# Performance work log

Hardware: AMD Instinct MI355X
Metric: run time of the kernel (lower is better)

Reference implementation:

```python
import jax, jax.numpy as jnp
import numpy as np
import math
from jax import lax

B, T, GS = 16, 511, 1
OBS, OUT = 60, 30
D, H, L = 1024, 16, 8
DFF, HID = 4096, 100
S = T + GS
DH = D // H
EPS = 1e-5


def _ln(x, g, b):
    m = jnp.mean(x, axis=-1, keepdims=True)
    v = jnp.mean(jnp.square(x - m), axis=-1, keepdims=True)
    return (x - m) * lax.rsqrt(v + EPS) * g + b


def setup_inputs():
    key = jax.random.key(0)
    ks = iter(jax.random.split(key, 32))
    def n(shape):
        return jax.random.normal(next(ks), shape, dtype=jnp.float32) * 0.02
    return {
        "states": jax.random.normal(next(ks), (B, T, OBS), dtype=jnp.float32),
        "goals": jax.random.normal(next(ks), (B, GS, OBS), dtype=jnp.float32),
        "Wtok": n((OBS, D)), "btok": jnp.zeros((D,), jnp.float32),
        "pos": n((1, S, D)),
        "ln1_g": jnp.ones((L, D), jnp.float32), "ln1_b": jnp.zeros((L, D), jnp.float32),
        "Wq": n((L, D, D)), "bq": jnp.zeros((L, D), jnp.float32),
        "Wk": n((L, D, D)), "bk": jnp.zeros((L, D), jnp.float32),
        "Wv": n((L, D, D)), "bv": jnp.zeros((L, D), jnp.float32),
        "Wp": n((L, D, D)), "bp": jnp.zeros((L, D), jnp.float32),
        "ln2_g": jnp.ones((L, D), jnp.float32), "ln2_b": jnp.zeros((L, D), jnp.float32),
        "Wm1": n((L, D, DFF)), "bm1": jnp.zeros((L, DFF), jnp.float32),
        "Wm2": n((L, DFF, D)), "bm2": jnp.zeros((L, D), jnp.float32),
        "lnf_g": jnp.ones((D,), jnp.float32), "lnf_b": jnp.zeros((D,), jnp.float32),
        "Wh1": n((D, HID)), "bh1": jnp.zeros((HID,), jnp.float32),
        "Wh2": n((HID, OUT)), "bh2": jnp.zeros((OUT,), jnp.float32),
    }


def reference(states, goals, Wtok, btok, pos, ln1_g, ln1_b, Wq, bq, Wk, bk, Wv, bv, Wp, bp,
              ln2_g, ln2_b, Wm1, bm1, Wm2, bm2, lnf_g, lnf_b, Wh1, bh1, Wh2, bh2):
    # token + positional embeddings (dropout is identity in eval mode, pdrop=0)
    goal_x = goals @ Wtok + btok + pos[:, :GS]
    state_x = states @ Wtok + btok + pos[:, GS:S]
    x = jnp.concatenate([goal_x, state_x], axis=1)  # (B, S, D)
    mask = jnp.tril(jnp.ones((S, S), dtype=bool))
    scale = 1.0 / math.sqrt(DH)

    def block(x, p):
        g1, b1, wq, bq_, wk, bk_, wv, bv_, wp, bp_, g2, b2, w1, bm1_, w2, bm2_ = p
        h = _ln(x, g1, b1)
        q = (h @ wq + bq_).reshape(B, S, H, DH).transpose(0, 2, 1, 3)  # (B,H,S,DH)
        k = (h @ wk + bk_).reshape(B, S, H, DH).transpose(0, 2, 1, 3)
        v = (h @ wv + bv_).reshape(B, S, H, DH).transpose(0, 2, 1, 3)
        att = jnp.einsum('bhqd,bhkd->bhqk', q, k) * scale
        att = jnp.where(mask, att, -jnp.inf)
        att = jax.nn.softmax(att, axis=-1)
        y = jnp.einsum('bhqk,bhkd->bhqd', att, v)
        y = y.transpose(0, 2, 1, 3).reshape(B, S, D) @ wp + bp_
        x = x + y
        h = _ln(x, g2, b2)
        x = x + (jax.nn.gelu(h @ w1 + bm1_, approximate=False) @ w2 + bm2_)
        return x, None

    x, _ = lax.scan(block, x, (ln1_g, ln1_b, Wq, bq, Wk, bk, Wv, bv, Wp, bp,
                               ln2_g, ln2_b, Wm1, bm1, Wm2, bm2))
    x = _ln(x, lnf_g, lnf_b)[:, GS:]  # drop goal tokens -> (B, T, D)
    h = jax.nn.silu(x @ Wh1 + bh1)
    return h @ Wh2 + bh2
```

## Files before the change

### kernel.cpp

```cpp
#include <hip/hip_runtime.h>
#include <cstdint>
#include <math.h>

#define NB_B   16
#define NB_T   511
#define NB_S   512
#define NB_OBS 60
#define NB_D   1024
#define NB_H   16
#define NB_L   8
#define NB_DFF 4096
#define NB_HID 100
#define NB_OUT 30
#define NB_M   8192
#define QKV_S  3072

typedef __attribute__((ext_vector_type(8))) short  short8;
typedef __attribute__((ext_vector_type(4))) short  short4v;
typedef __attribute__((ext_vector_type(4))) float  f32x4;
typedef __attribute__((ext_vector_type(8))) __bf16 bf16x8;

template <int N_> struct ic { static constexpr int v = N_; };

__device__ __forceinline__ short f2bf(float f) {
  union { float f; unsigned u; } a; a.f = f;
  unsigned u = a.u + 0x7fffu + ((a.u >> 16) & 1u);
  return (short)(u >> 16);
}

__device__ __forceinline__ void load_lds16(const void* g, void* l) {
  __builtin_amdgcn_global_load_lds(
      (__attribute__((address_space(1))) unsigned int*)(uintptr_t)g,
      (__attribute__((address_space(3))) unsigned int*)(unsigned)(uintptr_t)l,
      16, 0, 0);
}

__device__ __forceinline__ f32x4 mfma16(short8 a, short8 b, f32x4 c) {
  return __builtin_amdgcn_mfma_f32_16x16x32_bf16(
      __builtin_bit_cast(bf16x8, a), __builtin_bit_cast(bf16x8, b), c, 0, 0, 0);
}

__device__ __forceinline__ float gelu_fast(float v) {
  const float t = 1.5957691216057308f * (v + 0.044715f * v * v * v);
  const float e = __expf(fminf(t, 30.f));
  return v * (e / (e + 1.f));
}

__global__ __launch_bounds__(256) void tconv2_kernel(
    const float* __restrict__ src, short* __restrict__ dst,
    int R, int C, size_t sstride, size_t dstride) {
  __shared__ float t[64][65];
  const float* s0 = src + blockIdx.z * sstride;
  short* d0 = dst + blockIdx.z * dstride;
  const int c0 = blockIdx.x * 64, r0 = blockIdx.y * 64;
#pragma unroll
  for (int i = 0; i < 4; i++) {
    const int idx = threadIdx.x + i * 256;
    const int r = idx >> 4, c4 = (idx & 15) * 4;
    const float4 v = *(const float4*)&s0[(size_t)(r0 + r) * C + c0 + c4];
    t[r][c4 + 0] = v.x; t[r][c4 + 1] = v.y; t[r][c4 + 2] = v.z; t[r][c4 + 3] = v.w;
  }
  __syncthreads();
#pragma unroll
  for (int i = 0; i < 2; i++) {
    const int idx = threadIdx.x + i * 256;
    const int c = idx >> 3, g = (idx & 7) * 8;
    short8 o;
#pragma unroll
    for (int j = 0; j < 8; j++) o[j] = f2bf(t[g + j][c]);
    *(short8*)&d0[(size_t)(c0 + c) * R + r0 + g] = o;
  }
}

__global__ __launch_bounds__(256) void whead_prep(
    const float* __restrict__ Wh1, const float* __restrict__ bh1,
    short* __restrict__ Wh1t, float* __restrict__ bh1p) {
  const int idx = blockIdx.x * 256 + threadIdx.x;
  const int n = idx >> 10, k = idx & 1023;
  Wh1t[idx] = (n < NB_HID) ? f2bf(Wh1[k * NB_HID + n]) : (short)0;
  if (idx < 128) bh1p[idx] = (idx < NB_HID) ? bh1[idx] : 0.f;
}

__global__ __launch_bounds__(256) void qkvbias_prep(
    const float* __restrict__ bq, const float* __restrict__ bk,
    const float* __restrict__ bv, float* __restrict__ outb) {
  const int idx = blockIdx.x * 256 + threadIdx.x;
  const int l = idx / QKV_S, r = idx - l * QKV_S;
  const int z = r >> 10, c = r & 1023;
  const float* src = (z == 0) ? bq : ((z == 1) ? bk : bv);
  outb[idx] = src[l * NB_D + c];
}

__global__ __launch_bounds__(256) void embed2_kernel(
    const float* __restrict__ states, const float* __restrict__ goals,
    const float* __restrict__ Wtok, const float* __restrict__ btok,
    const float* __restrict__ pos, float* __restrict__ x) {
  const int r0 = blockIdx.x * 8;
  __shared__ float tok[8][NB_OBS];
  for (int idx = threadIdx.x; idx < 8 * NB_OBS; idx += 256) {
    const int r = idx / NB_OBS, o = idx - r * NB_OBS;
    const int row = r0 + r, b = row >> 9, s = row & 511;
    tok[r][o] = (s == 0) ? goals[b * NB_OBS + o]
                         : states[((size_t)b * NB_T + (s - 1)) * NB_OBS + o];
  }
  __syncthreads();
#pragma unroll
  for (int i = 0; i < 4; i++) {
    const int d = threadIdx.x + i * 256;
    float acc[8];
#pragma unroll
    for (int r = 0; r < 8; r++) acc[r] = 0.f;
    for (int o = 0; o < NB_OBS; o++) {
      const float wv = Wtok[o * NB_D + d];
#pragma unroll
      for (int r = 0; r < 8; r++) acc[r] += tok[r][o] * wv;
    }
    const float bt = btok[d];
#pragma unroll
    for (int r = 0; r < 8; r++) {
      const int row = r0 + r, s = row & 511;
      x[(size_t)row * NB_D + d] = acc[r] + bt + pos[(size_t)s * NB_D + d];
    }
  }
}

template <typename OutT>
__global__ __launch_bounds__(256) void ln_wave(
    const float* __restrict__ xin, const float* __restrict__ gam,
    const float* __restrict__ bet, OutT* __restrict__ outp) {
  const int row = blockIdx.x * 4 + (threadIdx.x >> 6);
  const int lane = threadIdx.x & 63;
  const float4* src = (const float4*)(xin + (size_t)row * NB_D);
  float4 v[4];
  float s = 0.f, s2 = 0.f;
#pragma unroll
  for (int i = 0; i < 4; i++) {
    v[i] = src[lane + 64 * i];
    s += v[i].x + v[i].y + v[i].z + v[i].w;
    s2 += v[i].x * v[i].x + v[i].y * v[i].y + v[i].z * v[i].z + v[i].w * v[i].w;
  }
#pragma unroll
  for (int o = 32; o; o >>= 1) {
    s += __shfl_xor(s, o, 64);
    s2 += __shfl_xor(s2, o, 64);
  }
  const float mean = s * (1.f / NB_D);
  const float var = s2 * (1.f / NB_D) - mean * mean;
  const float rs = rsqrtf(var + 1e-5f);
#pragma unroll
  for (int i = 0; i < 4; i++) {
    const float4 g4 = ((const float4*)gam)[lane + 64 * i];
    const float4 b4 = ((const float4*)bet)[lane + 64 * i];
    const float o0 = (v[i].x - mean) * rs * g4.x + b4.x;
    const float o1 = (v[i].y - mean) * rs * g4.y + b4.y;
    const float o2 = (v[i].z - mean) * rs * g4.z + b4.z;
    const float o3 = (v[i].w - mean) * rs * g4.w + b4.w;
    if constexpr (sizeof(OutT) == 2) {
      short4v r = {f2bf(o0), f2bf(o1), f2bf(o2), f2bf(o3)};
      *(short4v*)((short*)outp + (size_t)row * NB_D + (lane + 64 * i) * 4) = r;
    } else {
      ((float4*)((float*)outp + (size_t)row * NB_D))[lane + 64 * i] =
          make_float4(o0, o1, o2, o3);
    }
  }
}

template <int ACT, bool RESID, typename OutT>
__global__ __launch_bounds__(256) void gemm_bt(
    const short* __restrict__ A, const short* __restrict__ Bt,
    const float* __restrict__ bias, const float* __restrict__ resid,
    OutT* __restrict__ C, int N, int K) {
  __shared__ short As[128][32];
  __shared__ short Bs[128][32];
  const int bm = blockIdx.y * 128, bn = blockIdx.x * 128;
  const int tid = threadIdx.x;
  const int w = tid >> 6, lane = tid & 63;
  const int wr = (w >> 1) * 64, wc = (w & 1) * 64;
  const int rr = lane & 15, sg = lane >> 4;

  f32x4 acc[4][4];
#pragma unroll
  for (int i = 0; i < 4; i++)
#pragma unroll
    for (int j = 0; j < 4; j++) acc[i][j] = f32x4{0.f, 0.f, 0.f, 0.f};

  const int srow0 = w * 32 + (lane >> 2);
  const int sslot = lane & 3;

  for (int k0 = 0; k0 < K; k0 += 32) {
    __syncthreads();
#pragma unroll
    for (int inst = 0; inst < 2; inst++) {
      const int r = srow0 + inst * 16;
      const int sl = sslot ^ ((r >> 1) & 3);
      load_lds16(A + (size_t)(bm + r) * K + k0 + sl * 8, &As[w * 32 + inst * 16][0]);
      load_lds16(Bt + (size_t)(bn + r) * K + k0 + sl * 8, &Bs[w * 32 + inst * 16][0]);
    }
    __syncthreads();
    short8 a[4], b[4];
#pragma unroll
    for (int i = 0; i < 4; i++) {
      const int r = wr + i * 16 + rr;
      a[i] = *(const short8*)&As[r][(sg ^ ((r >> 1) & 3)) * 8];
      const int c = wc + i * 16 + rr;
      b[i] = *(const short8*)&Bs[c][(sg ^ ((c >> 1) & 3)) * 8];
    }
#pragma unroll
    for (int i = 0; i < 4; i++)
#pragma unroll
      for (int j = 0; j < 4; j++) acc[i][j] = mfma16(a[i], b[j], acc[i][j]);
  }

#pragma unroll
  for (int j = 0; j < 4; j++) {
    const int col = bn + wc + j * 16 + rr;
    const float bv = bias[col];
#pragma unroll
    for (int i = 0; i < 4; i++) {
#pragma unroll
      for (int q = 0; q < 4; q++) {
        const int row = bm + wr + i * 16 + sg * 4 + q;
        float v = acc[i][j][q] + bv;
        if constexpr (RESID) v += resid[(size_t)row * N + col];
        if constexpr (ACT == 1) v = gelu_fast(v);
        if constexpr (ACT == 2) v = v / (1.f + __expf(-v));
        if constexpr (sizeof(OutT) == 2) C[(size_t)row * N + col] = (OutT)f2bf(v);
        else C[(size_t)row * N + col] = v;
      }
    }
  }
}

template <int BM, int N, int K, int ACT, bool RESID, typename OutT>
__device__ __forceinline__ void gemmv4_core(
    const short* __restrict__ A, const short* __restrict__ Bt,
    const float* __restrict__ bias, const float* __restrict__ resid,
    OutT* __restrict__ C) {
  constexpr int MI = BM / 32;
  constexpr int NK = K / 32;
  constexpr int NBN = N / 128;
  constexpr int NWG = (NB_M / BM) * NBN;
  constexpr int QC = NWG / 8;
  constexpr int L = 2 + BM / 64;
  constexpr int SA = BM * 32;

  __shared__ short As[3][SA];
  __shared__ short Bs[3][128 * 32];

  int wg = blockIdx.x;
  wg = (wg & 7) * QC + (wg >> 3);
  const int bm = (wg / NBN) * BM;
  const int bn = (wg % NBN) * 128;

  const int tid = threadIdx.x;
  const int w = tid >> 6, lane = tid & 63;
  const int wm = w >> 1, wn = w & 1;
  const int rr = lane & 15, sg = lane >> 4;
  const int lrow = lane >> 2, lslot = lane & 3;
  const int sslot = lslot ^ ((lrow >> 1) & 3);

  const short* Asrc = A + (size_t)(bm + w * 16 + lrow) * K + sslot * 8;
  const short* Bsrc = Bt + (size_t)(bn + w * 16 + lrow) * K + sslot * 8;
  short* Adst = &As[0][w * 512];
  short* Bdst = &Bs[0][w * 512];

  const int ar = wm * (BM / 2) + rr;
  const int br = wn * 64 + rr;
  const int aoff = ar * 32 + ((sg ^ ((ar >> 1) & 3)) * 8);
  const int boff = br * 32 + ((sg ^ ((br >> 1) & 3)) * 8);

  f32x4 acc[MI][4];
#pragma unroll
  for (int i = 0; i < MI; i++)
#pragma unroll
    for (int j = 0; j < 4; j++) acc[i][j] = f32x4{0.f, 0.f, 0.f, 0.f};

  auto stage = [&](int sb, int k0) {
    load_lds16(Bsrc + k0,                  Bdst + sb * 4096);
    load_lds16(Bsrc + (size_t)64 * K + k0, Bdst + sb * 4096 + 2048);
#pragma unroll
    for (int c = 0; c < BM / 64; c++)
      load_lds16(Asrc + (size_t)(c * 64) * K + k0, Adst + sb * SA + c * 2048);
  };

  auto gate = [&]() {
    if constexpr (L == 6) asm volatile("s_waitcnt vmcnt(6)" ::: "memory");
    else                  asm volatile("s_waitcnt vmcnt(4)" ::: "memory");
  };

  stage(0, 0);
  stage(1, 32);
  gate();
  __builtin_amdgcn_s_barrier();

  auto ktile = [&](auto BUFC, auto SBUFC, int t) {
    constexpr int BUF = decltype(BUFC)::v;
    constexpr int SBUF = decltype(SBUFC)::v;
    const short* Ab = &As[BUF][0];
    const short* Bb = &Bs[BUF][0];
    if (t + 2 < NK) stage(SBUF, (t + 2) * 32);
    short8 a[MI], b[4];
#pragma unroll
    for (int i = 0; i < MI; i++) a[i] = *(const short8*)(Ab + aoff + i * 512);
#pragma unroll
    for (int j = 0; j < 4; j++) b[j] = *(const short8*)(Bb + boff + j * 512);
    __builtin_amdgcn_s_setprio(1);
#pragma unroll
    for (int i = 0; i < MI; i++)
#pragma unroll
      for (int j = 0; j < 4; j++) acc[i][j] = mfma16(a[i], b[j], acc[i][j]);
    __builtin_amdgcn_s_setprio(0);
    if (t + 2 < NK)      gate();
    else if (t + 1 < NK) asm volatile("s_waitcnt vmcnt(0)" ::: "memory");
    __builtin_amdgcn_s_barrier();
  };

  int t = 0;
#pragma unroll 1
  for (; t + 3 <= NK; t += 3) {
    ktile(ic<0>{}, ic<2>{}, t);
    ktile(ic<1>{}, ic<0>{}, t + 1);
    ktile(ic<2>{}, ic<1>{}, t + 2);
  }
  if constexpr (NK % 3 >= 1) ktile(ic<0>{}, ic<2>{}, NK - NK % 3);
  if constexpr (NK % 3 >= 2) ktile(ic<1>{}, ic<0>{}, NK - NK % 3 + 1);

  const int col0 = bn + wn * 64 + rr;
  float bv[4];
#pragma unroll
  for (int j = 0; j < 4; j++) bv[j] = bias[col0 + j * 16];
#pragma unroll
  for (int i = 0; i < MI; i++) {
#pragma unroll
    for (int q = 0; q < 4; q++) {
      const size_t row = bm + wm * (BM / 2) + i * 16 + sg * 4 + q;
      float v0 = acc[i][0][q] + bv[0];
      float v1 = acc[i][1][q] + bv[1];
      float v2 = acc[i][2][q] + bv[2];
      float v3 = acc[i][3][q] + bv[3];
      if constexpr (RESID) {
        const float* rrow = resid + row * N + col0;
        v0 += rrow[0]; v1 += rrow[16]; v2 += rrow[32]; v3 += rrow[48];
      }
      if constexpr (ACT == 1) {
        v0 = gelu_fast(v0); v1 = gelu_fast(v1);
        v2 = gelu_fast(v2); v3 = gelu_fast(v3);
      }
      OutT* crow = C + row * N + col0;
      if constexpr (sizeof(OutT) == 2) {
        crow[0] = (OutT)f2bf(v0); crow[16] = (OutT)f2bf(v1);
        crow[32] = (OutT)f2bf(v2); crow[48] = (OutT)f2bf(v3);
      } else {
        crow[0] = v0; crow[16] = v1; crow[32] = v2; crow[48] = v3;
      }
    }
  }
}

template <int BM, int N, int K, int ACT, bool RESID, typename OutT>
__global__ __launch_bounds__(256, 2) void gemmv4(
    const short* __restrict__ A, const short* __restrict__ Bt,
    const float* __restrict__ bias, const float* __restrict__ resid,
    OutT* __restrict__ C) {
  gemmv4_core<BM, N, K, ACT, RESID, OutT>(A, Bt, bias, resid, C);
}

__global__ __launch_bounds__(256) void attn_kernel(
    const short* __restrict__ qkv, short* __restrict__ out) {
  const int qt = blockIdx.x, hh = blockIdx.y, bb = blockIdx.z;
  const int tid = threadIdx.x;
  const int w = tid >> 6, lane = tid & 63;
  const int rr = lane & 15, sg = lane >> 4;

  __shared__ short Ks[64][64];
  __shared__ short Vt[64][64];
  __shared__ short Ps[4][16][64];

  short8 qf[2];
  {
    const size_t qrow = (size_t)bb * NB_S + qt * 64 + w * 16 + rr;
#pragma unroll
    for (int ks = 0; ks < 2; ks++)
      qf[ks] = *(const short8*)&qkv[qrow * QKV_S + hh * 64 + ks * 32 + sg * 8];
  }

  float mrow[4], lrow[4];
  f32x4 o[4];
#pragma unroll
  for (int j = 0; j < 4; j++) { mrow[j] = -INFINITY; lrow[j] = 0.f; }
#pragma unroll
  for (int nb = 0; nb < 4; nb++) o[nb] = f32x4{0.f, 0.f, 0.f, 0.f};

  for (int kt = 0; kt <= qt; kt++) {
    __syncthreads();
    {
      const int p = lane & 7;
#pragma unroll
      for (int inst = 0; inst < 2; inst++) {
        const int r = w * 16 + inst * 8 + (lane >> 3);
        const int sl = p ^ (r & 7);
        load_lds16(qkv + ((size_t)bb * NB_S + kt * 64 + r) * QKV_S + 1024 + hh * 64 + sl * 8,
                   &Ks[w * 16 + inst * 8][0]);
      }
    }
    {
#pragma unroll
      for (int cc = 0; cc < 2; cc++) {
        const int c = tid * 2 + cc;
        const int sk = c >> 3, sl = c & 7;
        short8 vv = *(const short8*)&qkv[((size_t)bb * NB_S + kt * 64 + sk) * QKV_S + 2048 + hh * 64 + sl * 8];
        const int ss = sk >> 3;
#pragma unroll
        for (int j = 0; j < 8; j++) {
          const int dh = sl * 8 + j;
          Vt[dh][(ss ^ (dh & 7)) * 8 + (sk & 7)] = vv[j];
        }
      }
    }
    __syncthreads();

    f32x4 sf[4];
#pragma unroll
    for (int nb = 0; nb < 4; nb++) sf[nb] = f32x4{0.f, 0.f, 0.f, 0.f};
#pragma unroll
    for (int ks = 0; ks < 2; ks++) {
#pragma unroll
      for (int nb = 0; nb < 4; nb++) {
        const int ck = nb * 16 + rr;
        short8 kf = *(const short8*)&Ks[ck][((ks * 4 + sg) ^ (ck & 7)) * 8];
        sf[nb] = mfma16(qf[ks], kf, sf[nb]);
      }
    }
    const int rbase = qt * 64 + w * 16 + sg * 4;
    float pmax[4] = {-INFINITY, -INFINITY, -INFINITY, -INFINITY};
#pragma unroll
    for (int nb = 0; nb < 4; nb++) {
      const int cg = kt * 64 + nb * 16 + rr;
#pragma unroll
      for (int j = 0; j < 4; j++) {
        float sv = sf[nb][j] * 0.125f;
        if (cg > rbase + j) sv = -INFINITY;
        sf[nb][j] = sv;
        pmax[j] = fmaxf(pmax[j], sv);
      }
    }
#pragma unroll
    for (int o1 = 1; o1 < 16; o1 <<= 1)
#pragma unroll
      for (int j = 0; j < 4; j++)
        pmax[j] = fmaxf(pmax[j], __shfl_xor(pmax[j], o1, 64));

    float resc[4], psum[4];
#pragma unroll
    for (int j = 0; j < 4; j++) {
      const float mn = fmaxf(mrow[j], pmax[j]);
      resc[j] = __expf(mrow[j] - mn);
      mrow[j] = mn;
      psum[j] = 0.f;
    }
#pragma unroll
    for (int nb = 0; nb < 4; nb++)
#pragma unroll
      for (int j = 0; j < 4; j++) {
        const float p = __expf(sf[nb][j] - mrow[j]);
        sf[nb][j] = p;
        psum[j] += p;
      }
#pragma unroll
    for (int o1 = 1; o1 < 16; o1 <<= 1)
#pragma unroll
      for (int j = 0; j < 4; j++) psum[j] += __shfl_xor(psum[j], o1, 64);
#pragma unroll
    for (int j = 0; j < 4; j++) lrow[j] = lrow[j] * resc[j] + psum[j];
#pragma unroll
    for (int nb = 0; nb < 4; nb++)
#pragma unroll
      for (int j = 0; j < 4; j++) o[nb][j] *= resc[j];

#pragma unroll
    for (int nb = 0; nb < 4; nb++) {
      const int ck = nb * 16 + rr;
      const int ss = ck >> 3;
#pragma unroll
      for (int j = 0; j < 4; j++) {
        const int rq = sg * 4 + j;
        Ps[w][rq][(ss ^ (rq & 7)) * 8 + (ck & 7)] = f2bf(sf[nb][j]);
      }
    }
#pragma unroll
    for (int ks = 0; ks < 2; ks++) {
      short8 pf = *(const short8*)&Ps[w][rr][((ks * 4 + sg) ^ (rr & 7)) * 8];
#pragma unroll
      for (int nb = 0; nb < 4; nb++) {
        const int dh = nb * 16 + rr;
        short8 vf = *(const short8*)&Vt[dh][((ks * 4 + sg) ^ (dh & 7)) * 8];
        o[nb] = mfma16(pf, vf, o[nb]);
      }
    }
  }

  {
    const size_t orow0 = (size_t)bb * NB_S + qt * 64 + w * 16;
#pragma unroll
    for (int nb = 0; nb < 4; nb++)
#pragma unroll
      for (int j = 0; j < 4; j++) {
        const float v = o[nb][j] / lrow[j];
        out[(orow0 + sg * 4 + j) * NB_D + hh * 64 + nb * 16 + rr] = f2bf(v);
      }
  }
}

__global__ __launch_bounds__(256) void head2_kernel(
    const float* __restrict__ hbuf, const float* __restrict__ Wh2,
    const float* __restrict__ bh2, float* __restrict__ outp) {
  __shared__ float hs[8][NB_HID];
  const int g0 = blockIdx.x * 8;
  for (int idx = threadIdx.x; idx < 8 * NB_HID; idx += 256) {
    const int r = idx / NB_HID, k = idx - r * NB_HID;
    const int gt = g0 + r;
    const int b = gt / NB_T, tt = gt - b * NB_T;
    hs[r][k] = hbuf[(size_t)(b * NB_S + 1 + tt) * 128 + k];
  }
  __syncthreads();
  const int r = threadIdx.x >> 5, c = threadIdx.x & 31;
  if (c < NB_OUT) {
    float acc = bh2[c];
#pragma unroll
    for (int k = 0; k < NB_HID; k++) acc += hs[r][k] * Wh2[k * NB_OUT + c];
    outp[(size_t)(g0 + r) * NB_OUT + c] = acc;
  }
}

extern "C" void kernel_launch(void* const* d_in, const int* in_sizes, int n_in,
                              void* d_out, int out_size, void* d_ws, size_t ws_size,
                              hipStream_t stream) {
  const float* states = (const float*)d_in[0];
  const float* goals  = (const float*)d_in[1];
  const float* Wtok   = (const float*)d_in[2];
  const float* btok   = (const float*)d_in[3];
  const float* pos    = (const float*)d_in[4];
  const float* ln1_g  = (const float*)d_in[5];
  const float* ln1_b  = (const float*)d_in[6];
  const float* Wq     = (const float*)d_in[7];
  const float* bq     = (const float*)d_in[8];
  const float* Wk     = (const float*)d_in[9];
  const float* bk     = (const float*)d_in[10];
  const float* Wv     = (const float*)d_in[11];
  const float* bv     = (const float*)d_in[12];
  const float* Wp     = (const float*)d_in[13];
  const float* bp     = (const float*)d_in[14];
  const float* ln2_g  = (const float*)d_in[15];
  const float* ln2_b  = (const float*)d_in[16];
  const float* Wm1    = (const float*)d_in[17];
  const float* bm1    = (const float*)d_in[18];
  const float* Wm2    = (const float*)d_in[19];
  const float* bm2    = (const float*)d_in[20];
  const float* lnf_g  = (const float*)d_in[21];
  const float* lnf_b  = (const float*)d_in[22];
  const float* Wh1    = (const float*)d_in[23];
  const float* bh1    = (const float*)d_in[24];
  const float* Wh2    = (const float*)d_in[25];
  const float* bh2    = (const float*)d_in[26];

  char* wsp = (char*)d_ws;
  size_t off = 0;
  auto carve = [&](size_t bytes) -> char* {
    char* p = wsp + off;
    off += (bytes + 1023) & ~(size_t)1023;
    return p;
  };
  short* Wqkv_t = (short*)carve((size_t)NB_L * 3 * NB_D * NB_D * 2);
  short* Wp_t   = (short*)carve((size_t)NB_L * NB_D * NB_D * 2);
  short* Wm1_t  = (short*)carve((size_t)NB_L * NB_DFF * NB_D * 2);
  short* Wm2_t  = (short*)carve((size_t)NB_L * NB_D * NB_DFF * 2);
  float* x      = (float*)carve((size_t)NB_M * NB_D * 4);
  short* h      = (short*)carve((size_t)NB_M * NB_D * 2);
  short* qkvb   = (short*)carve((size_t)NB_M * QKV_S * 2);
  short* mlp    = (short*)carve((size_t)NB_M * NB_DFF * 2);
  short* Wh1t   = (short*)carve((size_t)128 * NB_D * 2);
  float* bh1p   = (float*)carve(128 * 4);
  float* bqkv   = (float*)carve((size_t)NB_L * QKV_S * 4);
  short* attout = mlp;
  float* hbuf   = (float*)qkvb;

  const dim3 thr(256);
  const size_t DD = (size_t)NB_D * NB_D;
  const size_t DF = (size_t)NB_D * NB_DFF;

  tconv2_kernel<<<dim3(16, 16, NB_L), thr, 0, stream>>>(Wq, Wqkv_t + 0 * DD, NB_D, NB_D, DD, 3 * DD);
  tconv2_kernel<<<dim3(16, 16, NB_L), thr, 0, stream>>>(Wk, Wqkv_t + 1 * DD, NB_D, NB_D, DD, 3 * DD);
  tconv2_kernel<<<dim3(16, 16, NB_L), thr, 0, stream>>>(Wv, Wqkv_t + 2 * DD, NB_D, NB_D, DD, 3 * DD);
  tconv2_kernel<<<dim3(16, 16, NB_L), thr, 0, stream>>>(Wp, Wp_t, NB_D, NB_D, DD, DD);
  tconv2_kernel<<<dim3(64, 16, NB_L), thr, 0, stream>>>(Wm1, Wm1_t, NB_D, NB_DFF, DF, DF);
  tconv2_kernel<<<dim3(16, 64, NB_L), thr, 0, stream>>>(Wm2, Wm2_t, NB_DFF, NB_D, DF, DF);
  whead_prep<<<512, thr, 0, stream>>>(Wh1, bh1, Wh1t, bh1p);
  qkvbias_prep<<<96, thr, 0, stream>>>(bq, bk, bv, bqkv);

  embed2_kernel<<<NB_M / 8, thr, 0, stream>>>(states, goals, Wtok, btok, pos, x);

  for (int l = 0; l < NB_L; l++) {
    ln_wave<short><<<NB_M / 4, thr, 0, stream>>>(x, ln1_g + l * NB_D, ln1_b + l * NB_D, h);
    gemmv4<256, QKV_S, NB_D, 0, false, short><<<768, thr, 0, stream>>>(
        h, Wqkv_t + (size_t)l * 3 * DD, bqkv + (size_t)l * QKV_S, nullptr, qkvb);
    attn_kernel<<<dim3(NB_S / 64, NB_H, NB_B), thr, 0, stream>>>(qkvb, attout);
    gemmv4<128, NB_D, NB_D, 0, true, float><<<512, thr, 0, stream>>>(
        attout, Wp_t + (size_t)l * DD, bp + l * NB_D, x, x);
    ln_wave<short><<<NB_M / 4, thr, 0, stream>>>(x, ln2_g + l * NB_D, ln2_b + l * NB_D, h);
    gemmv4<256, NB_DFF, NB_D, 1, false, short><<<1024, thr, 0, stream>>>(
        h, Wm1_t + (size_t)l * DF, bm1 + l * NB_DFF, nullptr, mlp);
    gemmv4<128, NB_D, NB_DFF, 0, true, float><<<512, thr, 0, stream>>>(
        mlp, Wm2_t + (size_t)l * DF, bm2 + l * NB_D, x, x);
  }

  ln_wave<short><<<NB_M / 4, thr, 0, stream>>>(x, lnf_g, lnf_b, h);
  gemm_bt<2, false, float><<<dim3(1, NB_M / 128), thr, 0, stream>>>(
      h, Wh1t, bh1p, nullptr, hbuf, 128, NB_D);
  head2_kernel<<<NB_M / 8, thr, 0, stream>>>(hbuf, Wh2, bh2, (float*)d_out);
}
```

Measured before the change: 2.872 ms.

## Process 128 query rows per attention block to reuse K/V tiles

```diff
diff --git a/kernel.cpp b/kernel.cpp
--- a/kernel.cpp
+++ b/kernel.cpp
@@ -165,6 +165,140 @@
   }
 }
 
+template <int BM, int N, int K, int ACT, bool RESID, typename OutT>
+__device__ __forceinline__ void gemmv4_core(
+    const short* __restrict__ A, const short* __restrict__ Bt,
+    const float* __restrict__ bias, const float* __restrict__ resid,
+    OutT* __restrict__ C) {
+  constexpr int MI = BM / 32;
+  constexpr int NK = K / 32;
+  constexpr int NBN = N / 128;
+  constexpr int NWG = (NB_M / BM) * NBN;
+  constexpr int QC = NWG / 8;
+  constexpr int L = 2 + BM / 64;
+  constexpr int SA = BM * 32;
+
+  __shared__ short As[3][SA];
+  __shared__ short Bs[3][128 * 32];
+
+  int wg = blockIdx.x;
+  wg = (wg & 7) * QC + (wg >> 3);
+  const int bm = (wg / NBN) * BM;
+  const int bn = (wg % NBN) * 128;
+
+  const int tid = threadIdx.x;
+  const int w = tid >> 6, lane = tid & 63;
+  const int wm = w >> 1, wn = w & 1;
+  const int rr = lane & 15, sg = lane >> 4;
+  const int lrow = lane >> 2, lslot = lane & 3;
+  const int sslot = lslot ^ ((lrow >> 1) & 3);
+
+  const short* Asrc = A + (size_t)(bm + w * 16 + lrow) * K + sslot * 8;
+  const short* Bsrc = Bt + (size_t)(bn + w * 16 + lrow) * K + sslot * 8;
+  short* Adst = &As[0][w * 512];
+  short* Bdst = &Bs[0][w * 512];
+
+  const int ar = wm * (BM / 2) + rr;
+  const int br = wn * 64 + rr;
+  const int aoff = ar * 32 + ((sg ^ ((ar >> 1) & 3)) * 8);
+  const int boff = br * 32 + ((sg ^ ((br >> 1) & 3)) * 8);
+
+  f32x4 acc[MI][4];
+#pragma unroll
+  for (int i = 0; i < MI; i++)
+#pragma unroll
+    for (int j = 0; j < 4; j++) acc[i][j] = f32x4{0.f, 0.f, 0.f, 0.f};
+
+  auto stage = [&](int sb, int k0) {
+    load_lds16(Bsrc + k0,                  Bdst + sb * 4096);
+    load_lds16(Bsrc + (size_t)64 * K + k0, Bdst + sb * 4096 + 2048);
+#pragma unroll
+    for (int c = 0; c < BM / 64; c++)
+      load_lds16(Asrc + (size_t)(c * 64) * K + k0, Adst + sb * SA + c * 2048);
+  };
+
+  auto gate = [&]() {
+    if constexpr (L == 6) asm volatile("s_waitcnt vmcnt(6)" ::: "memory");
+    else                  asm volatile("s_waitcnt vmcnt(4)" ::: "memory");
+  };
+
+  stage(0, 0);
+  stage(1, 32);
+  gate();
+  __builtin_amdgcn_s_barrier();
+
+  auto ktile = [&](auto BUFC, auto SBUFC, int t) {
+    constexpr int BUF = decltype(BUFC)::v;
+    constexpr int SBUF = decltype(SBUFC)::v;
+    const short* Ab = &As[BUF][0];
+    const short* Bb = &Bs[BUF][0];
+    if (t + 2 < NK) stage(SBUF, (t + 2) * 32);
+    short8 a[MI], b[4];
+#pragma unroll
+    for (int i = 0; i < MI; i++) a[i] = *(const short8*)(Ab + aoff + i * 512);
+#pragma unroll
+    for (int j = 0; j < 4; j++) b[j] = *(const short8*)(Bb + boff + j * 512);
+    __builtin_amdgcn_s_setprio(1);
+#pragma unroll
+    for (int i = 0; i < MI; i++)
+#pragma unroll
+      for (int j = 0; j < 4; j++) acc[i][j] = mfma16(a[i], b[j], acc[i][j]);
+    __builtin_amdgcn_s_setprio(0);
+    if (t + 2 < NK)      gate();
+    else if (t + 1 < NK) asm volatile("s_waitcnt vmcnt(0)" ::: "memory");
+    __builtin_amdgcn_s_barrier();
+  };
+
+  int t = 0;
+#pragma unroll 1
+  for (; t + 3 <= NK; t += 3) {
+    ktile(ic<0>{}, ic<2>{}, t);
+    ktile(ic<1>{}, ic<0>{}, t + 1);
+    ktile(ic<2>{}, ic<1>{}, t + 2);
+  }
+  if constexpr (NK % 3 >= 1) ktile(ic<0>{}, ic<2>{}, NK - NK % 3);
+  if constexpr (NK % 3 >= 2) ktile(ic<1>{}, ic<0>{}, NK - NK % 3 + 1);
+
+  const int col0 = bn + wn * 64 + rr;
+  float bv[4];
+#pragma unroll
+  for (int j = 0; j < 4; j++) bv[j] = bias[col0 + j * 16];
+#pragma unroll
+  for (int i = 0; i < MI; i++) {
+#pragma unroll
+    for (int q = 0; q < 4; q++) {
+      const size_t row = bm + wm * (BM / 2) + i * 16 + sg * 4 + q;
+      float v0 = acc[i][0][q] + bv[0];
+      float v1 = acc[i][1][q] + bv[1];
+      float v2 = acc[i][2][q] + bv[2];
+      float v3 = acc[i][3][q] + bv[3];
+      if constexpr (RESID) {
+        const float* rrow = resid + row * N + col0;
+        v0 += rrow[0]; v1 += rrow[16]; v2 += rrow[32]; v3 += rrow[48];
+      }
+      if constexpr (ACT == 1) {
+        v0 = gelu_fast(v0); v1 = gelu_fast(v1);
+        v2 = gelu_fast(v2); v3 = gelu_fast(v3);
+      }
+      OutT* crow = C + row * N + col0;
+      if constexpr (sizeof(OutT) == 2) {
+        crow[0] = (OutT)f2bf(v0); crow[16] = (OutT)f2bf(v1);
+        crow[32] = (OutT)f2bf(v2); crow[48] = (OutT)f2bf(v3);
+      } else {
+        crow[0] = v0; crow[16] = v1; crow[32] = v2; crow[48] = v3;
+      }
+    }
+  }
+}
+
+template <int BM, int N, int K, int ACT, bool RESID, typename OutT>
+__global__ __launch_bounds__(256, 2) void gemmv4(
+    const short* __restrict__ A, const short* __restrict__ Bt,
+    const float* __restrict__ bias, const float* __restrict__ resid,
+    OutT* __restrict__ C) {
+  gemmv4_core<BM, N, K, ACT, RESID, OutT>(A, Bt, bias, resid, C);
+}
+
 template <int ACT, bool RESID, typename OutT>
 __global__ __launch_bounds__(256) void gemm_bt(
     const short* __restrict__ A, const short* __restrict__ Bt,
@@ -231,141 +365,7 @@
   }
 }
 
-template <int BM, int N, int K, int ACT, bool RESID, typename OutT>
-__device__ __forceinline__ void gemmv4_core(
-    const short* __restrict__ A, const short* __restrict__ Bt,
-    const float* __restrict__ bias, const float* __restrict__ resid,
-    OutT* __restrict__ C) {
-  constexpr int MI = BM / 32;
-  constexpr int NK = K / 32;
-  constexpr int NBN = N / 128;
-  constexpr int NWG = (NB_M / BM) * NBN;
-  constexpr int QC = NWG / 8;
-  constexpr int L = 2 + BM / 64;
-  constexpr int SA = BM * 32;
-
-  __shared__ short As[3][SA];
-  __shared__ short Bs[3][128 * 32];
-
-  int wg = blockIdx.x;
-  wg = (wg & 7) * QC + (wg >> 3);
-  const int bm = (wg / NBN) * BM;
-  const int bn = (wg % NBN) * 128;
-
-  const int tid = threadIdx.x;
-  const int w = tid >> 6, lane = tid & 63;
-  const int wm = w >> 1, wn = w & 1;
-  const int rr = lane & 15, sg = lane >> 4;
-  const int lrow = lane >> 2, lslot = lane & 3;
-  const int sslot = lslot ^ ((lrow >> 1) & 3);
-
-  const short* Asrc = A + (size_t)(bm + w * 16 + lrow) * K + sslot * 8;
-  const short* Bsrc = Bt + (size_t)(bn + w * 16 + lrow) * K + sslot * 8;
-  short* Adst = &As[0][w * 512];
-  short* Bdst = &Bs[0][w * 512];
-
-  const int ar = wm * (BM / 2) + rr;
-  const int br = wn * 64 + rr;
-  const int aoff = ar * 32 + ((sg ^ ((ar >> 1) & 3)) * 8);
-  const int boff = br * 32 + ((sg ^ ((br >> 1) & 3)) * 8);
-
-  f32x4 acc[MI][4];
-#pragma unroll
-  for (int i = 0; i < MI; i++)
-#pragma unroll
-    for (int j = 0; j < 4; j++) acc[i][j] = f32x4{0.f, 0.f, 0.f, 0.f};
-
-  auto stage = [&](int sb, int k0) {
-    load_lds16(Bsrc + k0,                  Bdst + sb * 4096);
-    load_lds16(Bsrc + (size_t)64 * K + k0, Bdst + sb * 4096 + 2048);
-#pragma unroll
-    for (int c = 0; c < BM / 64; c++)
-      load_lds16(Asrc + (size_t)(c * 64) * K + k0, Adst + sb * SA + c * 2048);
-  };
-
-  auto gate = [&]() {
-    if constexpr (L == 6) asm volatile("s_waitcnt vmcnt(6)" ::: "memory");
-    else                  asm volatile("s_waitcnt vmcnt(4)" ::: "memory");
-  };
-
-  stage(0, 0);
-  stage(1, 32);
-  gate();
-  __builtin_amdgcn_s_barrier();
-
-  auto ktile = [&](auto BUFC, auto SBUFC, int t) {
-    constexpr int BUF = decltype(BUFC)::v;
-    constexpr int SBUF = decltype(SBUFC)::v;
-    const short* Ab = &As[BUF][0];
-    const short* Bb = &Bs[BUF][0];
-    if (t + 2 < NK) stage(SBUF, (t + 2) * 32);
-    short8 a[MI], b[4];
-#pragma unroll
-    for (int i = 0; i < MI; i++) a[i] = *(const short8*)(Ab + aoff + i * 512);
-#pragma unroll
-    for (int j = 0; j < 4; j++) b[j] = *(const short8*)(Bb + boff + j * 512);
-    __builtin_amdgcn_s_setprio(1);
-#pragma unroll
-    for (int i = 0; i < MI; i++)
-#pragma unroll
-      for (int j = 0; j < 4; j++) acc[i][j] = mfma16(a[i], b[j], acc[i][j]);
-    __builtin_amdgcn_s_setprio(0);
-    if (t + 2 < NK)      gate();
-    else if (t + 1 < NK) asm volatile("s_waitcnt vmcnt(0)" ::: "memory");
-    __builtin_amdgcn_s_barrier();
-  };
-
-  int t = 0;
-#pragma unroll 1
-  for (; t + 3 <= NK; t += 3) {
-    ktile(ic<0>{}, ic<2>{}, t);
-    ktile(ic<1>{}, ic<0>{}, t + 1);
-    ktile(ic<2>{}, ic<1>{}, t + 2);
-  }
-  if constexpr (NK % 3 >= 1) ktile(ic<0>{}, ic<2>{}, NK - NK % 3);
-  if constexpr (NK % 3 >= 2) ktile(ic<1>{}, ic<0>{}, NK - NK % 3 + 1);
-
-  const int col0 = bn + wn * 64 + rr;
-  float bv[4];
-#pragma unroll
-  for (int j = 0; j < 4; j++) bv[j] = bias[col0 + j * 16];
-#pragma unroll
-  for (int i = 0; i < MI; i++) {
-#pragma unroll
-    for (int q = 0; q < 4; q++) {
-      const size_t row = bm + wm * (BM / 2) + i * 16 + sg * 4 + q;
-      float v0 = acc[i][0][q] + bv[0];
-      float v1 = acc[i][1][q] + bv[1];
-      float v2 = acc[i][2][q] + bv[2];
-      float v3 = acc[i][3][q] + bv[3];
-      if constexpr (RESID) {
-        const float* rrow = resid + row * N + col0;
-        v0 += rrow[0]; v1 += rrow[16]; v2 += rrow[32]; v3 += rrow[48];
-      }
-      if constexpr (ACT == 1) {
-        v0 = gelu_fast(v0); v1 = gelu_fast(v1);
-        v2 = gelu_fast(v2); v3 = gelu_fast(v3);
-      }
-      OutT* crow = C + row * N + col0;
-      if constexpr (sizeof(OutT) == 2) {
-        crow[0] = (OutT)f2bf(v0); crow[16] = (OutT)f2bf(v1);
-        crow[32] = (OutT)f2bf(v2); crow[48] = (OutT)f2bf(v3);
-      } else {
-        crow[0] = v0; crow[16] = v1; crow[32] = v2; crow[48] = v3;
-      }
-    }
-  }
-}
-
-template <int BM, int N, int K, int ACT, bool RESID, typename OutT>
-__global__ __launch_bounds__(256, 2) void gemmv4(
-    const short* __restrict__ A, const short* __restrict__ Bt,
-    const float* __restrict__ bias, const float* __restrict__ resid,
-    OutT* __restrict__ C) {
-  gemmv4_core<BM, N, K, ACT, RESID, OutT>(A, Bt, bias, resid, C);
-}
-
-__global__ __launch_bounds__(256) void attn_kernel(
+__global__ __launch_bounds__(256) void attn2_kernel(
     const short* __restrict__ qkv, short* __restrict__ out) {
   const int qt = blockIdx.x, hh = blockIdx.y, bb = blockIdx.z;
   const int tid = threadIdx.x;
@@ -376,22 +376,29 @@
   __shared__ short Vt[64][64];
   __shared__ short Ps[4][16][64];
 
-  short8 qf[2];
-  {
-    const size_t qrow = (size_t)bb * NB_S + qt * 64 + w * 16 + rr;
+  const int qrow_base = qt * 128 + w * 32;
+
+  short8 qf[2][2];
+#pragma unroll
+  for (int g = 0; g < 2; g++) {
+    const size_t qrow = (size_t)bb * NB_S + qrow_base + g * 16 + rr;
 #pragma unroll
     for (int ks = 0; ks < 2; ks++)
-      qf[ks] = *(const short8*)&qkv[qrow * QKV_S + hh * 64 + ks * 32 + sg * 8];
-  }
-
-  float mrow[4], lrow[4];
-  f32x4 o[4];
-#pragma unroll
-  for (int j = 0; j < 4; j++) { mrow[j] = -INFINITY; lrow[j] = 0.f; }
-#pragma unroll
-  for (int nb = 0; nb < 4; nb++) o[nb] = f32x4{0.f, 0.f, 0.f, 0.f};
-
-  for (int kt = 0; kt <= qt; kt++) {
+      qf[g][ks] = *(const short8*)&qkv[qrow * QKV_S + hh * 64 + ks * 32 + sg * 8];
+  }
+
+  float mrow[2][4], lrow[2][4];
+  f32x4 o[2][4];
+#pragma unroll
+  for (int g = 0; g < 2; g++)
+#pragma unroll
+    for (int j = 0; j < 4; j++) {
+      mrow[g][j] = -INFINITY; lrow[g][j] = 0.f;
+      o[g][j] = f32x4{0.f, 0.f, 0.f, 0.f};
+    }
+
+  const int ktmax = 2 * qt + 1;
+  for (int kt = 0; kt <= ktmax; kt++) {
     __syncthreads();
     {
       const int p = lane & 7;
@@ -419,93 +426,99 @@
     }
     __syncthreads();
 
-    f32x4 sf[4];
-#pragma unroll
-    for (int nb = 0; nb < 4; nb++) sf[nb] = f32x4{0.f, 0.f, 0.f, 0.f};
-#pragma unroll
-    for (int ks = 0; ks < 2; ks++) {
+#pragma unroll
+    for (int g = 0; g < 2; g++) {
+      if (kt * 64 > qrow_base + g * 16 + 15) continue;
+
+      f32x4 sf[4];
+#pragma unroll
+      for (int nb = 0; nb < 4; nb++) sf[nb] = f32x4{0.f, 0.f, 0.f, 0.f};
+#pragma unroll
+      for (int ks = 0; ks < 2; ks++) {
+#pragma unroll
+        for (int nb = 0; nb < 4; nb++) {
+          const int ck = nb * 16 + rr;
+          short8 kf = *(const short8*)&Ks[ck][((ks * 4 + sg) ^ (ck & 7)) * 8];
+          sf[nb] = mfma16(qf[g][ks], kf, sf[nb]);
+        }
+      }
+      const int rbase = qrow_base + g * 16 + sg * 4;
+      float pmax[4] = {-INFINITY, -INFINITY, -INFINITY, -INFINITY};
+#pragma unroll
+      for (int nb = 0; nb < 4; nb++) {
+        const int cg = kt * 64 + nb * 16 + rr;
+#pragma unroll
+        for (int j = 0; j < 4; j++) {
+          float sv = sf[nb][j] * 0.125f;
+          if (cg > rbase + j) sv = -INFINITY;
+          sf[nb][j] = sv;
+          pmax[j] = fmaxf(pmax[j], sv);
+        }
+      }
+#pragma unroll
+      for (int o1 = 1; o1 < 16; o1 <<= 1)
+#pragma unroll
+        for (int j = 0; j < 4; j++)
+          pmax[j] = fmaxf(pmax[j], __shfl_xor(pmax[j], o1, 64));
+
+      float resc[4], psum[4];
+#pragma unroll
+      for (int j = 0; j < 4; j++) {
+        const float mn = fmaxf(mrow[g][j], pmax[j]);
+        resc[j] = __expf(mrow[g][j] - mn);
+        mrow[g][j] = mn;
+        psum[j] = 0.f;
+      }
+#pragma unroll
+      for (int nb = 0; nb < 4; nb++)
+#pragma unroll
+        for (int j = 0; j < 4; j++) {
+          const float p = __expf(sf[nb][j] - mrow[g][j]);
+          sf[nb][j] = p;
+          psum[j] += p;
+        }
+#pragma unroll
+      for (int o1 = 1; o1 < 16; o1 <<= 1)
+#pragma unroll
+        for (int j = 0; j < 4; j++) psum[j] += __shfl_xor(psum[j], o1, 64);
+#pragma unroll
+      for (int j = 0; j < 4; j++) lrow[g][j] = lrow[g][j] * resc[j] + psum[j];
+#pragma unroll
+      for (int nb = 0; nb < 4; nb++)
+#pragma unroll
+        for (int j = 0; j < 4; j++) o[g][nb][j] *= resc[j];
+
 #pragma unroll
       for (int nb = 0; nb < 4; nb++) {
         const int ck = nb * 16 + rr;
-        short8 kf = *(const short8*)&Ks[ck][((ks * 4 + sg) ^ (ck & 7)) * 8];
-        sf[nb] = mfma16(qf[ks], kf, sf[nb]);
-      }
-    }
-    const int rbase = qt * 64 + w * 16 + sg * 4;
-    float pmax[4] = {-INFINITY, -INFINITY, -INFINITY, -INFINITY};
-#pragma unroll
-    for (int nb = 0; nb < 4; nb++) {
-      const int cg = kt * 64 + nb * 16 + rr;
+        const int ss = ck >> 3;
+#pragma unroll
+        for (int j = 0; j < 4; j++) {
+          const int rq = sg * 4 + j;
+          Ps[w][rq][(ss ^ (rq & 7)) * 8 + (ck & 7)] = f2bf(sf[nb][j]);
+        }
+      }
+#pragma unroll
+      for (int ks = 0; ks < 2; ks++) {
+        short8 pf = *(const short8*)&Ps[w][rr][((ks * 4 + sg) ^ (rr & 7)) * 8];
+#pragma unroll
+        for (int nb = 0; nb < 4; nb++) {
+          const int dh = nb * 16 + rr;
+          short8 vf = *(const short8*)&Vt[dh][((ks * 4 + sg) ^ (dh & 7)) * 8];
+          o[g][nb] = mfma16(pf, vf, o[g][nb]);
+        }
+      }
+    }
+  }
+
+#pragma unroll
+  for (int g = 0; g < 2; g++) {
+    const size_t orow0 = (size_t)bb * NB_S + qrow_base + g * 16;
+#pragma unroll
+    for (int nb = 0; nb < 4; nb++)
 #pragma unroll
       for (int j = 0; j < 4; j++) {
-        float sv = sf[nb][j] * 0.125f;
-        if (cg > rbase + j) sv = -INFINITY;
-        sf[nb][j] = sv;
-        pmax[j] = fmaxf(pmax[j], sv);
-      }
-    }
-#pragma unroll
-    for (int o1 = 1; o1 < 16; o1 <<= 1)
-#pragma unroll
-      for (int j = 0; j < 4; j++)
-        pmax[j] = fmaxf(pmax[j], __shfl_xor(pmax[j], o1, 64));
-
-    float resc[4], psum[4];
-#pragma unroll
-    for (int j = 0; j < 4; j++) {
-      const float mn = fmaxf(mrow[j], pmax[j]);
-      resc[j] = __expf(mrow[j] - mn);
-      mrow[j] = mn;
-      psum[j] = 0.f;
-    }
-#pragma unroll
-    for (int nb = 0; nb < 4; nb++)
-#pragma unroll
-      for (int j = 0; j < 4; j++) {
-        const float p = __expf(sf[nb][j] - mrow[j]);
-        sf[nb][j] = p;
-        psum[j] += p;
-      }
-#pragma unroll
-    for (int o1 = 1; o1 < 16; o1 <<= 1)
-#pragma unroll
-      for (int j = 0; j < 4; j++) psum[j] += __shfl_xor(psum[j], o1, 64);
-#pragma unroll
-    for (int j = 0; j < 4; j++) lrow[j] = lrow[j] * resc[j] + psum[j];
-#pragma unroll
-    for (int nb = 0; nb < 4; nb++)
-#pragma unroll
-      for (int j = 0; j < 4; j++) o[nb][j] *= resc[j];
-
-#pragma unroll
-    for (int nb = 0; nb < 4; nb++) {
-      const int ck = nb * 16 + rr;
-      const int ss = ck >> 3;
-#pragma unroll
-      for (int j = 0; j < 4; j++) {
-        const int rq = sg * 4 + j;
-        Ps[w][rq][(ss ^ (rq & 7)) * 8 + (ck & 7)] = f2bf(sf[nb][j]);
-      }
-    }
-#pragma unroll
-    for (int ks = 0; ks < 2; ks++) {
-      short8 pf = *(const short8*)&Ps[w][rr][((ks * 4 + sg) ^ (rr & 7)) * 8];
-#pragma unroll
-      for (int nb = 0; nb < 4; nb++) {
-        const int dh = nb * 16 + rr;
-        short8 vf = *(const short8*)&Vt[dh][((ks * 4 + sg) ^ (dh & 7)) * 8];
-        o[nb] = mfma16(pf, vf, o[nb]);
-      }
-    }
-  }
-
-  {
-    const size_t orow0 = (size_t)bb * NB_S + qt * 64 + w * 16;
-#pragma unroll
-    for (int nb = 0; nb < 4; nb++)
-#pragma unroll
-      for (int j = 0; j < 4; j++) {
-        const float v = o[nb][j] / lrow[j];
+        const float v = o[g][nb][j] / lrow[g][j];
         out[(orow0 + sg * 4 + j) * NB_D + hh * 64 + nb * 16 + rr] = f2bf(v);
       }
   }
@@ -603,7 +616,7 @@
     ln_wave<short><<<NB_M / 4, thr, 0, stream>>>(x, ln1_g + l * NB_D, ln1_b + l * NB_D, h);
     gemmv4<256, QKV_S, NB_D, 0, false, short><<<768, thr, 0, stream>>>(
         h, Wqkv_t + (size_t)l * 3 * DD, bqkv + (size_t)l * QKV_S, nullptr, qkvb);
-    attn_kernel<<<dim3(NB_S / 64, NB_H, NB_B), thr, 0, stream>>>(qkvb, attout);
+    attn2_kernel<<<dim3(NB_S / 128, NB_H, NB_B), thr, 0, stream>>>(qkvb, attout);
     gemmv4<128, NB_D, NB_D, 0, true, float><<<512, thr, 0, stream>>>(
         attout, Wp_t + (size_t)l * DD, bp + l * NB_D, x, x);
     ln_wave<short><<<NB_M / 4, thr, 0, stream>>>(x, ln2_g + l * NB_D, ln2_b + l * NB_D, h);
```

New measurement: 2.844 ms. Within noise of the previous version (-1.0%).
